# Kernel optimization log

Hardware: AMD Instinct MI355X
Metric: run time of the kernel (lower is better)

## Reference

```python
import jax, jax.numpy as jnp
import numpy as np

EMBED_DIM = 768
NUM_HEADS = 12
HEAD_DIM = EMBED_DIM // NUM_HEADS


def setup_inputs() -> dict:
    key = jax.random.key(0)
    k1, k2, k3, k4, k5 = jax.random.split(key, 5)
    x = jax.random.normal(k1, (2, 4096, EMBED_DIM), dtype=jnp.float32)
    # nn.Linear(embedding_dim, 3*embedding_dim): weight [3d, d], bias [3d]
    w_qkv = jax.random.normal(k2, (3 * EMBED_DIM, EMBED_DIM), dtype=jnp.float32) * (1.0 / np.sqrt(EMBED_DIM))
    b_qkv = jax.random.normal(k3, (3 * EMBED_DIM,), dtype=jnp.float32) * 0.02
    # LayerNorm affine params
    ln_gamma = jnp.ones((EMBED_DIM,), dtype=jnp.float32)
    ln_beta = jnp.zeros((EMBED_DIM,), dtype=jnp.float32)
    return {"x": x, "w_qkv": w_qkv, "b_qkv": b_qkv, "ln_gamma": ln_gamma, "ln_beta": ln_beta}


def _layernorm(x, gamma, beta, eps=1e-5):
    mu = jnp.mean(x, axis=-1, keepdims=True)
    var = jnp.var(x, axis=-1, keepdims=True)
    return (x - mu) * jax.lax.rsqrt(var + eps) * gamma + beta


def reference(x, w_qkv, b_qkv, ln_gamma, ln_beta):
    b, n, d = x.shape
    h, hd = NUM_HEADS, HEAD_DIM
    qkv = x @ w_qkv.T + b_qkv                      # [b, n, 3d]
    qkv = qkv.reshape(b, n, 3, h, hd)
    qkv = jnp.transpose(qkv, (2, 0, 3, 1, 4))      # [3, b, h, n, hd]
    Q, K, V = qkv[0], qkv[1], qkv[2]
    scale = 1.0 / np.sqrt(hd).astype(np.float32)
    scores = jnp.einsum('bhqd,bhkd->bhqk', Q, K) * scale   # [b, h, n, n]
    attn = jax.nn.softmax(scores, axis=-1)
    out = jnp.einsum('bhqk,bhkd->bhqd', attn, V)           # [b, h, n, hd]
    out = jnp.transpose(out, (0, 2, 1, 3)).reshape(b, n, d)
    return _layernorm(x + out, ln_gamma, ln_beta)
```

## Files before the change

### kernel.cpp

```cpp
#include <hip/hip_runtime.h>
#include <stdint.h>

#define NUM_HEADS 12
#define HEAD_DIM 64
#define EMB 768
#define SEQ 4096
#define BATCH 2
#define ROWS (BATCH*SEQ)
#define DQKV (3*EMB)

typedef __attribute__((ext_vector_type(8))) __bf16 bf16x8;
typedef __attribute__((ext_vector_type(4))) float floatx4;

static __device__ __forceinline__ unsigned short f2bf(float f) {
  unsigned int u = __float_as_uint(f);
  u += 0x7FFFu + ((u >> 16) & 1u);
  return (unsigned short)(u >> 16);
}

static __device__ __forceinline__ float bf2f(unsigned short h) {
  return __uint_as_float(((unsigned int)h) << 16);
}

static __device__ __forceinline__ unsigned int pack_bf2_trunc(float a, float b) {
  return __builtin_amdgcn_perm(__float_as_uint(b), __float_as_uint(a), 0x07060302u);
}

static __device__ __forceinline__ void async_cp16(void* lds, const void* g) {
  __builtin_amdgcn_global_load_lds(
      (__attribute__((address_space(1))) void*)(g),
      (__attribute__((address_space(3))) void*)(lds), 16, 0, 0);
}

static __device__ __forceinline__ int perm_key(int nn) {
  return (nn & ~31) | (((nn >> 2) & 3) * 8 + ((nn >> 4) & 1) * 4 + (nn & 3));
}

#define N4X (ROWS*EMB/4)
#define N4W (DQKV*EMB/4)
__global__ __launch_bounds__(256) void cvt2_kernel(
    const float* __restrict__ x, const float* __restrict__ w,
    unsigned short* __restrict__ xb, unsigned short* __restrict__ wb) {
  int i = blockIdx.x * blockDim.x + threadIdx.x;
  const float4* src;
  ushort4* dst;
  if (i < N4X) { src = (const float4*)x; dst = (ushort4*)xb; }
  else { i -= N4X; if (i >= N4W) return; src = (const float4*)w; dst = (ushort4*)wb; }
  float4 v = src[i];
  ushort4 o;
  o.x = f2bf(v.x); o.y = f2bf(v.y); o.z = f2bf(v.z); o.w = f2bf(v.w);
  dst[i] = o;
}

__global__ __launch_bounds__(256) void qkv_gemm_kernel(
    const unsigned short* __restrict__ xb, const unsigned short* __restrict__ wb,
    const float* __restrict__ bias,
    unsigned short* __restrict__ Qb, unsigned short* __restrict__ Kb,
    unsigned short* __restrict__ Vt) {
  __shared__ unsigned short As[128 * 64];
  __shared__ unsigned short Bs[128 * 64];
  const int t = threadIdx.x;
  const int lane = t & 63;
  const int w = t >> 6;
  const int wm = w >> 1, wn = w & 1;
  const int fr = lane & 15, fq = lane >> 4;
  const int fx = fr & 7;
  const int m0 = blockIdx.x * 128;
  const int n0 = blockIdx.y * 128;
  const int sel = n0 / EMB;
  const int lr = t >> 3;
  const int sc = t & 7;

  floatx4 acc[4][4];
#pragma unroll
  for (int i = 0; i < 4; ++i)
#pragma unroll
    for (int j = 0; j < 4; ++j) acc[i][j] = (floatx4)(0.0f);

  if (sel < 2) {
    for (int k0 = 0; k0 < EMB; k0 += 64) {
      __syncthreads();
#pragma unroll
      for (int i = 0; i < 4; ++i) {
        const int rr = i*32 + lr;
        const int cg = ((sc ^ (lr & 7)) * 8);
        async_cp16(&As[rr*64 + sc*8], &xb[(size_t)(m0 + rr)*EMB + k0 + cg]);
        async_cp16(&Bs[rr*64 + sc*8], &wb[(size_t)(n0 + rr)*EMB + k0 + cg]);
      }
      __syncthreads();
#pragma unroll
      for (int ks = 0; ks < 2; ++ks) {
        bf16x8 af[4], bfr[4];
#pragma unroll
        for (int i = 0; i < 4; ++i)
          af[i] = *(const bf16x8*)&As[(wm*64 + i*16 + fr)*64 + (((ks*4+fq) ^ fx)*8)];
#pragma unroll
        for (int j = 0; j < 4; ++j)
          bfr[j] = *(const bf16x8*)&Bs[(wn*64 + j*16 + fr)*64 + (((ks*4+fq) ^ fx)*8)];
#pragma unroll
        for (int i = 0; i < 4; ++i)
#pragma unroll
          for (int j = 0; j < 4; ++j)
            acc[i][j] = __builtin_amdgcn_mfma_f32_16x16x32_bf16(bfr[j], af[i], acc[i][j], 0, 0, 0);
      }
    }
    const float qscale = 0.125f * 1.4426950408889634f;
    const float sc2 = (sel == 0) ? qscale : 1.0f;
    unsigned short* dst = (sel == 0) ? Qb : Kb;
#pragma unroll
    for (int i = 0; i < 4; ++i) {
      const int mr = m0 + wm*64 + i*16 + fr;
      const int b = mr / SEQ;
      const int nn = mr - b*SEQ;
#pragma unroll
      for (int j = 0; j < 4; ++j) {
        const int og = n0 + wn*64 + j*16 + fq*4;
        const int oo = og - sel*EMB;
        const int hh = oo >> 6, dd = oo & 63;
        const float4 bv = *(const float4*)&bias[og];
        ushort4 pk;
        pk.x = f2bf((acc[i][j][0] + bv.x) * sc2);
        pk.y = f2bf((acc[i][j][1] + bv.y) * sc2);
        pk.z = f2bf((acc[i][j][2] + bv.z) * sc2);
        pk.w = f2bf((acc[i][j][3] + bv.w) * sc2);
        *(ushort4*)&dst[(((size_t)(b*NUM_HEADS + hh))*SEQ + nn)*HEAD_DIM + dd] = pk;
      }
    }
  } else {
    for (int k0 = 0; k0 < EMB; k0 += 64) {
      __syncthreads();
#pragma unroll
      for (int i = 0; i < 4; ++i) {
        const int rr = i*32 + lr;
        const int cg = ((sc ^ (lr & 7)) * 8);
        async_cp16(&As[rr*64 + sc*8], &xb[(size_t)(m0 + rr)*EMB + k0 + cg]);
        async_cp16(&Bs[rr*64 + sc*8], &wb[(size_t)(n0 + rr)*EMB + k0 + cg]);
      }
      __syncthreads();
#pragma unroll
      for (int ks = 0; ks < 2; ++ks) {
        bf16x8 af[4], bfr[4];
#pragma unroll
        for (int i = 0; i < 4; ++i)
          af[i] = *(const bf16x8*)&As[(wm*64 + i*16 + fr)*64 + (((ks*4+fq) ^ fx)*8)];
#pragma unroll
        for (int j = 0; j < 4; ++j)
          bfr[j] = *(const bf16x8*)&Bs[(wn*64 + j*16 + fr)*64 + (((ks*4+fq) ^ fx)*8)];
#pragma unroll
        for (int i = 0; i < 4; ++i)
#pragma unroll
          for (int j = 0; j < 4; ++j)
            acc[i][j] = __builtin_amdgcn_mfma_f32_16x16x32_bf16(af[i], bfr[j], acc[i][j], 0, 0, 0);
      }
    }
#pragma unroll
    for (int i = 0; i < 4; ++i) {
      const int mr = m0 + wm*64 + i*16 + fq*4;
      const int b = mr / SEQ;
      const int nn = perm_key(mr - b*SEQ);
#pragma unroll
      for (int j = 0; j < 4; ++j) {
        const int feat = n0 + wn*64 + j*16 + fr;
        const int oo = feat - 2*EMB;
        const int hh = oo >> 6, dd = oo & 63;
        const float bv = bias[feat];
        ushort4 pk;
        pk.x = f2bf(acc[i][j][0] + bv);
        pk.y = f2bf(acc[i][j][1] + bv);
        pk.z = f2bf(acc[i][j][2] + bv);
        pk.w = f2bf(acc[i][j][3] + bv);
        *(ushort4*)&Vt[(((size_t)(b*NUM_HEADS + hh))*HEAD_DIM + dd)*SEQ + nn] = pk;
      }
    }
  }
}

__global__ __launch_bounds__(256, 4) void attn_kernel(
    const unsigned short* __restrict__ Qb, const unsigned short* __restrict__ Kb,
    const unsigned short* __restrict__ Vt, unsigned short* __restrict__ Oo) {
  __shared__ unsigned short Ks[128 * 64];
  __shared__ unsigned short Vs[64 * 128];
  const int t = threadIdx.x;
  const int lane = t & 63;
  const int w = t >> 6;
  const int fr = lane & 15, fq = lane >> 4;
  const int fx = fr & 7;
  const int bh = blockIdx.y;
  const int q0 = blockIdx.x * 128 + w * 32;

  bf16x8 aq[2][2];
#pragma unroll
  for (int g = 0; g < 2; ++g) {
    const size_t qoff = ((size_t)bh * SEQ + q0 + g*16 + fr) * HEAD_DIM;
    aq[g][0] = *(const bf16x8*)&Qb[qoff + fq*8];
    aq[g][1] = *(const bf16x8*)&Qb[qoff + 32 + fq*8];
  }

  union { unsigned int u[4]; bf16x8 b; } onesu;
  onesu.u[0] = onesu.u[1] = onesu.u[2] = onesu.u[3] = 0x3F803F80u;
  const bf16x8 onesb = onesu.b;

  floatx4 o[2][4];
  floatx4 lsum[2];
#pragma unroll
  for (int g = 0; g < 2; ++g) {
    lsum[g] = (floatx4)(0.f);
#pragma unroll
    for (int d = 0; d < 4; ++d) o[g][d] = (floatx4)(0.f);
  }

  const size_t kb = (size_t)bh * SEQ * HEAD_DIM;
  const size_t vb = (size_t)bh * HEAD_DIM * SEQ;

  for (int kc = 0; kc < SEQ; kc += 128) {
    __syncthreads();
#pragma unroll
    for (int i = 0; i < 4; ++i) {
      const int chunk = i*256 + t;
      const int r = chunk >> 3, c = chunk & 7;
      async_cp16(&Ks[chunk*8], &Kb[kb + (size_t)(kc + r)*HEAD_DIM + ((c ^ (r&7))*8)]);
    }
#pragma unroll
    for (int i = 0; i < 4; ++i) {
      const int chunk = i*256 + t;
      const int r = chunk >> 4, c = chunk & 15;
      async_cp16(&Vs[chunk*8], &Vt[vb + (size_t)r*SEQ + kc + ((c ^ (r&7))*8)]);
    }
    __syncthreads();

#pragma unroll
    for (int J = 0; J < 4; ++J) {
      floatx4 z[2][2];
#pragma unroll
      for (int jj = 0; jj < 2; ++jj) {
        const int row = (J*2 + jj)*16 + fr;
        bf16x8 k0 = *(const bf16x8*)&Ks[row*64 + ((fq ^ fx)*8)];
        bf16x8 k1 = *(const bf16x8*)&Ks[row*64 + (((fq+4) ^ fx)*8)];
#pragma unroll
        for (int g = 0; g < 2; ++g) {
          floatx4 accz = (floatx4)(0.f);
          accz = __builtin_amdgcn_mfma_f32_16x16x32_bf16(k0, aq[g][0], accz, 0, 0, 0);
          accz = __builtin_amdgcn_mfma_f32_16x16x32_bf16(k1, aq[g][1], accz, 0, 0, 0);
          z[g][jj] = accz;
        }
      }
      bf16x8 ap[2];
#pragma unroll
      for (int g = 0; g < 2; ++g) {
        float e0 = __builtin_amdgcn_exp2f(z[g][0][0]);
        float e1 = __builtin_amdgcn_exp2f(z[g][0][1]);
        float e2 = __builtin_amdgcn_exp2f(z[g][0][2]);
        float e3 = __builtin_amdgcn_exp2f(z[g][0][3]);
        float e4 = __builtin_amdgcn_exp2f(z[g][1][0]);
        float e5 = __builtin_amdgcn_exp2f(z[g][1][1]);
        float e6 = __builtin_amdgcn_exp2f(z[g][1][2]);
        float e7 = __builtin_amdgcn_exp2f(z[g][1][3]);
        union { unsigned int u[4]; bf16x8 b; } cv;
        cv.u[0] = pack_bf2_trunc(e0, e1);
        cv.u[1] = pack_bf2_trunc(e2, e3);
        cv.u[2] = pack_bf2_trunc(e4, e5);
        cv.u[3] = pack_bf2_trunc(e6, e7);
        ap[g] = cv.b;
      }
#pragma unroll
      for (int g = 0; g < 2; ++g)
        lsum[g] = __builtin_amdgcn_mfma_f32_16x16x32_bf16(ap[g], onesb, lsum[g], 0, 0, 0);
#pragma unroll
      for (int dt = 0; dt < 4; ++dt) {
        const int r = dt*16 + fr;
        const bf16x8 vvb = *(const bf16x8*)&Vs[r*128 + (((4*J + fq) ^ fx)*8)];
#pragma unroll
        for (int g = 0; g < 2; ++g)
          o[g][dt] = __builtin_amdgcn_mfma_f32_16x16x32_bf16(ap[g], vvb, o[g][dt], 0, 0, 0);
      }
    }
  }

  const int b = bh / NUM_HEADS, hh = bh - b*NUM_HEADS;
#pragma unroll
  for (int g = 0; g < 2; ++g)
#pragma unroll
    for (int r4 = 0; r4 < 4; ++r4) {
      const float li = 1.0f / lsum[g][r4];
      const size_t obase = ((size_t)b*SEQ + q0 + g*16 + fq*4 + r4)*EMB + hh*HEAD_DIM;
#pragma unroll
      for (int dt = 0; dt < 4; ++dt)
        Oo[obase + dt*16 + fr] = f2bf(o[g][dt][r4] * li);
    }
}

__global__ __launch_bounds__(256) void ln_kernel(
    const float* __restrict__ x, const unsigned short* __restrict__ att,
    const float* __restrict__ gamma, const float* __restrict__ beta,
    float* __restrict__ out) {
  const int row = blockIdx.x * 4 + (threadIdx.x >> 6);
  const int lane = threadIdx.x & 63;
  const size_t base = (size_t)row * EMB;
  float4 v[3];
  float s = 0.f, s2 = 0.f;
#pragma unroll
  for (int k = 0; k < 3; ++k) {
    const int c = lane*4 + k*256;
    const float4 xv = *(const float4*)&x[base + c];
    const ushort4 a4 = *(const ushort4*)&att[base + c];
    v[k].x = xv.x + bf2f(a4.x);
    v[k].y = xv.y + bf2f(a4.y);
    v[k].z = xv.z + bf2f(a4.z);
    v[k].w = xv.w + bf2f(a4.w);
    s  += (v[k].x + v[k].y) + (v[k].z + v[k].w);
    s2 += (v[k].x*v[k].x + v[k].y*v[k].y) + (v[k].z*v[k].z + v[k].w*v[k].w);
  }
#pragma unroll
  for (int off = 1; off < 64; off <<= 1) {
    s  += __shfl_xor(s,  off);
    s2 += __shfl_xor(s2, off);
  }
  const float mean = s * (1.0f / EMB);
  const float var  = s2 * (1.0f / EMB) - mean * mean;
  const float rstd = rsqrtf(var + 1e-5f);
#pragma unroll
  for (int k = 0; k < 3; ++k) {
    const int c = lane*4 + k*256;
    const float4 g4 = *(const float4*)&gamma[c];
    const float4 b4 = *(const float4*)&beta[c];
    float4 ov;
    ov.x = (v[k].x - mean) * rstd * g4.x + b4.x;
    ov.y = (v[k].y - mean) * rstd * g4.y + b4.y;
    ov.z = (v[k].z - mean) * rstd * g4.z + b4.z;
    ov.w = (v[k].w - mean) * rstd * g4.w + b4.w;
    *(float4*)&out[base + c] = ov;
  }
}

extern "C" void kernel_launch(void* const* d_in, const int* in_sizes, int n_in,
                              void* d_out, int out_size, void* d_ws, size_t ws_size,
                              hipStream_t stream) {
  const float* x      = (const float*)d_in[0];
  const float* w_qkv  = (const float*)d_in[1];
  const float* b_qkv  = (const float*)d_in[2];
  const float* gamma  = (const float*)d_in[3];
  const float* beta   = (const float*)d_in[4];
  float* out = (float*)d_out;

  unsigned short* xb = (unsigned short*)d_ws;
  unsigned short* wb = xb + (size_t)ROWS * EMB;
  unsigned short* Qb = wb + (size_t)DQKV * EMB;
  unsigned short* Kb = Qb + (size_t)ROWS * EMB;
  unsigned short* Vt = Kb + (size_t)ROWS * EMB;
  unsigned short* att = Vt + (size_t)ROWS * EMB;

  cvt2_kernel<<<(N4X + N4W + 255)/256, 256, 0, stream>>>(x, w_qkv, xb, wb);
  qkv_gemm_kernel<<<dim3(ROWS/128, DQKV/128), 256, 0, stream>>>(xb, wb, b_qkv, Qb, Kb, Vt);
  attn_kernel<<<dim3(SEQ/128, BATCH*NUM_HEADS), 256, 0, stream>>>(Qb, Kb, Vt, att);
  ln_kernel<<<ROWS/4, 256, 0, stream>>>(x, att, gamma, beta, out);
}
```

Measured before the change: 247.3 us.

## Software-pipeline QK^T MFMAs ahead of softmax and split V tile in LDS

Inside the attention inner loop, the QK^T score fragments for the next 32-key sub-block are now computed before the exp/pack and PV MFMAs of the current one, so matrix work can overlap the transcendental and pack instructions. The V tile in LDS is reorganised into two 64x64 halves with 8-chunk XOR swizzle instead of one 64x128 tile, which changes the bank-conflict pattern of the V fragment reads. The cost is extra live registers for the prefetched score fragments, which may pressure occupancy under launch_bounds(256,4).

```diff
diff --git a/kernel.cpp b/kernel.cpp
--- a/kernel.cpp
+++ b/kernel.cpp
@@ -179,7 +179,7 @@
     const unsigned short* __restrict__ Qb, const unsigned short* __restrict__ Kb,
     const unsigned short* __restrict__ Vt, unsigned short* __restrict__ Oo) {
   __shared__ unsigned short Ks[128 * 64];
-  __shared__ unsigned short Vs[64 * 128];
+  __shared__ unsigned short Vs[2][64 * 64];
   const int t = threadIdx.x;
   const int lane = t & 63;
   const int w = t >> 6;
@@ -212,6 +212,22 @@
   const size_t kb = (size_t)bh * SEQ * HEAD_DIM;
   const size_t vb = (size_t)bh * HEAD_DIM * SEQ;
 
+  auto sfrag = [&](int J2, floatx4 zz[2][2]) {
+#pragma unroll
+    for (int jj = 0; jj < 2; ++jj) {
+      const int row = (J2*2 + jj)*16 + fr;
+      bf16x8 k0 = *(const bf16x8*)&Ks[row*64 + ((fq ^ fx)*8)];
+      bf16x8 k1 = *(const bf16x8*)&Ks[row*64 + (((fq+4) ^ fx)*8)];
+#pragma unroll
+      for (int g = 0; g < 2; ++g) {
+        floatx4 a = (floatx4)(0.f);
+        a = __builtin_amdgcn_mfma_f32_16x16x32_bf16(k0, aq[g][0], a, 0, 0, 0);
+        a = __builtin_amdgcn_mfma_f32_16x16x32_bf16(k1, aq[g][1], a, 0, 0, 0);
+        zz[g][jj] = a;
+      }
+    }
+  };
+
   for (int kc = 0; kc < SEQ; kc += 128) {
     __syncthreads();
 #pragma unroll
@@ -223,27 +239,19 @@
 #pragma unroll
     for (int i = 0; i < 4; ++i) {
       const int chunk = i*256 + t;
-      const int r = chunk >> 4, c = chunk & 15;
-      async_cp16(&Vs[chunk*8], &Vt[vb + (size_t)r*SEQ + kc + ((c ^ (r&7))*8)]);
+      const int h = chunk >> 9, rem = chunk & 511;
+      const int r = rem >> 3, c = rem & 7;
+      async_cp16(&Vs[0][0] + chunk*8,
+                 &Vt[vb + (size_t)r*SEQ + kc + h*64 + ((c ^ (r&7))*8)]);
     }
     __syncthreads();
 
+    floatx4 z[2][2];
+    sfrag(0, z);
 #pragma unroll
     for (int J = 0; J < 4; ++J) {
-      floatx4 z[2][2];
-#pragma unroll
-      for (int jj = 0; jj < 2; ++jj) {
-        const int row = (J*2 + jj)*16 + fr;
-        bf16x8 k0 = *(const bf16x8*)&Ks[row*64 + ((fq ^ fx)*8)];
-        bf16x8 k1 = *(const bf16x8*)&Ks[row*64 + (((fq+4) ^ fx)*8)];
-#pragma unroll
-        for (int g = 0; g < 2; ++g) {
-          floatx4 accz = (floatx4)(0.f);
-          accz = __builtin_amdgcn_mfma_f32_16x16x32_bf16(k0, aq[g][0], accz, 0, 0, 0);
-          accz = __builtin_amdgcn_mfma_f32_16x16x32_bf16(k1, aq[g][1], accz, 0, 0, 0);
-          z[g][jj] = accz;
-        }
-      }
+      floatx4 zn[2][2];
+      if (J < 3) sfrag(J+1, zn);
       bf16x8 ap[2];
 #pragma unroll
       for (int g = 0; g < 2; ++g) {
@@ -265,13 +273,20 @@
 #pragma unroll
       for (int g = 0; g < 2; ++g)
         lsum[g] = __builtin_amdgcn_mfma_f32_16x16x32_bf16(ap[g], onesb, lsum[g], 0, 0, 0);
+      const unsigned short* vsh = &Vs[J >> 1][0];
+      const int vc = ((4*(J & 1) + fq) ^ fx) * 8;
 #pragma unroll
       for (int dt = 0; dt < 4; ++dt) {
-        const int r = dt*16 + fr;
-        const bf16x8 vvb = *(const bf16x8*)&Vs[r*128 + (((4*J + fq) ^ fx)*8)];
+        const bf16x8 vvb = *(const bf16x8*)&vsh[(dt*16 + fr)*64 + vc];
 #pragma unroll
         for (int g = 0; g < 2; ++g)
           o[g][dt] = __builtin_amdgcn_mfma_f32_16x16x32_bf16(ap[g], vvb, o[g][dt], 0, 0, 0);
+      }
+      if (J < 3) {
+#pragma unroll
+        for (int g = 0; g < 2; ++g)
+#pragma unroll
+          for (int jj = 0; jj < 2; ++jj) z[g][jj] = zn[g][jj];
       }
     }
   }
```

New measurement: 245.9 us. Within noise of the previous version (-0.6%).
